# Optimization experiments

Hardware: AMD Instinct MI355X
Metric: run time of the kernel (lower is better)

Reference implementation:

```python
import jax, jax.numpy as jnp
import numpy as np

GROUPS = 4
KLD_SCALE = 10.0
COMMIT_COST = 0.25


def setup_inputs() -> dict:
    key = jax.random.key(0)
    k1, k2, k3, k4 = jax.random.split(key, 4)
    B, H, C = 8, 4096, 512
    n_embed, d = 512, C // GROUPS
    return {
        "z": jax.random.normal(k1, (B, H, C), dtype=jnp.float32),
        "embed_w": jax.random.normal(k2, (n_embed, d), dtype=jnp.float32),
        "proj_w": jax.random.normal(k3, (C, C), dtype=jnp.float32) * (1.0 / np.sqrt(C)),
        "proj_b": jax.random.normal(k4, (C,), dtype=jnp.float32) * 0.01,
    }


def reference(z, embed_w, proj_w, proj_b):
    B, H, C = z.shape
    d = C // GROUPS
    sg = jax.lax.stop_gradient
    # split channels into groups -> [B, H*groups, d]
    z_e = z.reshape(B, H * GROUPS, d)
    flat = z_e.reshape(-1, d)  # [N, d]
    dist = ((flat ** 2).sum(1, keepdims=True)
            - 2.0 * flat @ embed_w.T
            + (embed_w ** 2).sum(1)[None, :])  # [N, n_embed]
    ind = jnp.argmin(dist, axis=1).reshape(B, H * GROUPS)  # (-dist).max == dist.min
    z_q = embed_w[ind]  # [B, H*groups, d]
    diff = KLD_SCALE * (COMMIT_COST * jnp.mean((sg(z_q) - z_e) ** 2)
                        + jnp.mean((z_q - sg(z_e)) ** 2))
    # straight-through estimator
    z_q = z_e + sg(z_q - z_e)
    z_q = z_q.reshape(B, H, C)
    out = z_q @ proj_w.T + proj_b
    return out, diff, ind
```

## Files before the change

### kernel.cpp

```cpp
#include <hip/hip_runtime.h>

constexpr int D         = 128;
constexpr int NE        = 512;
constexpr int NROWS     = 131072;
constexpr int CC        = 512;
constexpr int OUT_ELEMS = 16777216;


using half8  = __attribute__((ext_vector_type(8))) _Float16;
using f32x16 = __attribute__((ext_vector_type(16))) float;

#define F16_MINNORM 6.103515625e-05f

__global__ void eprep_kernel(const float* __restrict__ embed,
                             unsigned short* __restrict__ esw,
                             float* __restrict__ entab,
                             float* __restrict__ ws_diff) {
    const int chunk = blockIdx.x;
    const int tid = threadIdx.x;
    const int cl = tid >> 3;
    const int seg = tid & 7;
    const float* src = embed + (size_t)(chunk * 32 + cl) * D + seg * 16;
    unsigned short* cb = esw + (size_t)chunk * 8192;

    float ss = 0.f;
#pragma unroll
    for (int g2 = 0; g2 < 2; g2++) {
        float4 a = ((const float4*)src)[g2 * 2 + 0];
        float4 b = ((const float4*)src)[g2 * 2 + 1];
        float v[8] = {a.x, a.y, a.z, a.w, b.x, b.y, b.z, b.w};
        half8 t1, t2;
#pragma unroll
        for (int i = 0; i < 8; i++) {
            ss += v[i] * v[i];
            float m2 = -2.0f * v[i];
            float m2c = (__builtin_fabsf(m2) < F16_MINNORM) ? 0.0f : m2;
            _Float16 h = (_Float16)m2c;
            float r = m2 - (float)h;
            t1[i] = h;
            t2[i] = (_Float16)(r * 2048.0f);
        }
        const int idx = seg * 512 + g2 * 256 + cl * 8;
        *(half8*)(cb + idx) = t1;
        *(half8*)(cb + 4096 + idx) = t2;
    }
    ss += __shfl_down(ss, 4, 8);
    ss += __shfl_down(ss, 2, 8);
    ss += __shfl_down(ss, 1, 8);
    if (seg == 0) entab[chunk * 32 + cl] = ss;
    if (chunk == 0 && tid == 0) ws_diff[0] = 0.0f;
}

#define AS_STRIDE 68
#define AS_S4 17

__launch_bounds__(256, 4)
__global__ void pgemm_kernel(const float* __restrict__ embed,
                             const float* __restrict__ projw,
                             float* __restrict__ P) {
    __shared__ float As[64 * AS_STRIDE];
    __shared__ float Bs[64 * AS_STRIDE];
    const int tid = threadIdx.x;
    const int cbase = blockIdx.x * 64;
    const int jbase = blockIdx.y * 64;
    const int g = blockIdx.z;
    const int tx = tid & 15, ty = tid >> 4;
    const int r = tid >> 2, seg = tid & 3;

    float acc[4][4];
#pragma unroll
    for (int i = 0; i < 4; i++)
#pragma unroll
        for (int j = 0; j < 4; j++) acc[i][j] = 0.f;

    for (int kb = 0; kb < D; kb += 64) {
        const float4* asrc = (const float4*)(embed + (size_t)(jbase + r) * D + kb + seg * 16);
        const float4* bsrc = (const float4*)(projw + (size_t)(cbase + r) * CC + g * D + kb + seg * 16);
        float4* adst = (float4*)&As[r * AS_STRIDE + seg * 16];
        float4* bdst = (float4*)&Bs[r * AS_STRIDE + seg * 16];
#pragma unroll
        for (int q = 0; q < 4; q++) { adst[q] = asrc[q]; bdst[q] = bsrc[q]; }
        __syncthreads();

        const float4* as4 = (const float4*)As;
        const float4* bs4 = (const float4*)Bs;
#pragma unroll 4
        for (int kk = 0; kk < 16; kk++) {
            float4 a[4], b[4];
#pragma unroll
            for (int i = 0; i < 4; i++) a[i] = as4[(ty + 16 * i) * AS_S4 + kk];
#pragma unroll
            for (int j = 0; j < 4; j++) b[j] = bs4[(tx + 16 * j) * AS_S4 + kk];
#pragma unroll
            for (int i = 0; i < 4; i++)
#pragma unroll
                for (int j = 0; j < 4; j++)
                    acc[i][j] += a[i].x * b[j].x + a[i].y * b[j].y +
                                 a[i].z * b[j].z + a[i].w * b[j].w;
        }
        __syncthreads();
    }
#pragma unroll
    for (int j = 0; j < 4; j++) {
#pragma unroll
        for (int i = 0; i < 4; i++)
            P[(size_t)g * 262144 + (size_t)(jbase + ty + 16 * i) * CC + cbase + tx + 16 * j] =
                acc[i][j];
    }
}

__global__ __launch_bounds__(256, 3)
void argmin_fused_kernel(const float* __restrict__ z,
                         const unsigned short* __restrict__ esw,
                         const float* __restrict__ entab,
                         const float* __restrict__ P,
                         const float* __restrict__ projb,
                         float* __restrict__ ws_diff,
                         float* __restrict__ ind_f,
                         float* __restrict__ out) {
    __shared__ unsigned char ebuf[32768];
    __shared__ int ind_s[128];
    const int tid = threadIdx.x;
    const int lane = tid & 63;
    const int wave = tid >> 6;
    const int h5 = lane >> 5, l5 = lane & 31;
    const int rb = blockIdx.x * 128 + wave * 32;

    half8 x1[8], x2[8];
    float xn = 0.f;
    {
        const float* zr = z + (size_t)(rb + l5) * D + h5 * 8;
#pragma unroll
        for (int kk = 0; kk < 8; kk++) {
            float4 a = *(const float4*)(zr + kk * 16);
            float4 b = *(const float4*)(zr + kk * 16 + 4);
            float v[8] = {a.x, a.y, a.z, a.w, b.x, b.y, b.z, b.w};
            half8 t1, t2;
#pragma unroll
            for (int i = 0; i < 8; i++) {
                xn += v[i] * v[i];
                float vc = (__builtin_fabsf(v[i]) < F16_MINNORM) ? 0.0f : v[i];
                _Float16 h = (_Float16)vc;
                float r = v[i] - (float)h;
                t1[i] = h;
                t2[i] = (_Float16)(r * 2048.0f);
            }
            x1[kk] = t1; x2[kk] = t2;
        }
    }

    float minv = 3.0e38f;
    int   mini = 0;

    auto stage = [&](int c, int b) {
        const unsigned char* s = (const unsigned char*)esw + (size_t)c * 16384 +
                                 wave * 4096 + lane * 16;
        unsigned char* d = &ebuf[b * 16384 + wave * 4096];
#pragma unroll
        for (int it = 0; it < 4; it++)
            __builtin_amdgcn_global_load_lds(
                (const __attribute__((address_space(1))) unsigned int*)(s + it * 1024),
                (__attribute__((address_space(3))) unsigned int*)(d + it * 1024),
                16, 0, 0);
    };

    stage(0, 0);
    __syncthreads();

#pragma unroll 1
    for (int c = 0; c < 16; c++) {
        if (c < 15) stage(c + 1, (c + 1) & 1);
        const unsigned char* ldsb = &ebuf[(c & 1) * 16384];

        float4 enr[4];
#pragma unroll
        for (int u = 0; u < 4; u++)
            enr[u] = *(const float4*)(entab + c * 32 + h5 * 4 + u * 8);

        f32x16 accA = (f32x16)(0.0f), accB = (f32x16)(0.0f);
#pragma unroll
        for (int kk = 0; kk < 8; kk++) {
            const int fo = kk * 1024 + h5 * 512 + l5 * 16;
            half8 e1 = *(const half8*)(ldsb + fo);
            half8 e2 = *(const half8*)(ldsb + 8192 + fo);
            accA = __builtin_amdgcn_mfma_f32_32x32x16_f16(e1, x1[kk], accA, 0, 0, 0);
            accB = __builtin_amdgcn_mfma_f32_32x32x16_f16(e1, x2[kk], accB, 0, 0, 0);
            accB = __builtin_amdgcn_mfma_f32_32x32x16_f16(e2, x1[kk], accB, 0, 0, 0);
        }

        const int cb2 = c * 32 + h5 * 4;
#pragma unroll
        for (int r = 0; r < 16; r++) {
            const float en = ((const float*)&enr[r >> 2])[r & 3];
            const int cand = cb2 + (r & 3) + 8 * (r >> 2);
            float d0 = fmaf(accB[r], 4.8828125e-4f, accA[r]) + en;
            if (d0 < minv) { minv = d0; mini = cand; }
        }
        __syncthreads();
    }

    {
        float ov = __shfl_xor(minv, 32);
        int oi = __shfl_xor(mini, 32);
        if (ov < minv || (ov == minv && oi < mini)) { minv = ov; mini = oi; }
    }
    if (lane < 32) {
        ind_f[rb + l5] = (float)mini;
        ind_s[wave * 32 + l5] = mini;
    }

    float xfull = xn + __shfl_xor(xn, 32);
    float v = (lane < 32) ? (xfull + minv) : 0.0f;
#pragma unroll
    for (int off = 32; off; off >>= 1) v += __shfl_down(v, off);
    if (lane == 0) atomicAdd(ws_diff, v);

    __syncthreads();

    const int mb = blockIdx.x * 32;
    const int c4 = tid & 127;
    const int mh = (tid >> 7) * 16;
    const float4 bias = ((const float4*)projb)[c4];
    const float4* P4 = (const float4*)P;
#pragma unroll 4
    for (int u = 0; u < 16; u++) {
        const int ml = mh + u;
        float4 acc = bias;
#pragma unroll
        for (int g = 0; g < 4; g++) {
            const int ig = ind_s[ml * 4 + g];
            float4 p = P4[(size_t)g * 65536 + (size_t)ig * 128 + c4];
            acc.x += p.x; acc.y += p.y; acc.z += p.z; acc.w += p.w;
        }
        ((float4*)out)[(size_t)(mb + ml) * 128 + c4] = acc;
    }
}

__global__ void finalize_kernel(const float* __restrict__ ws_diff,
                                float* __restrict__ diff_out) {
    diff_out[0] = 12.5f * ws_diff[0] * (1.0f / 16777216.0f);
}

extern "C" void kernel_launch(void* const* d_in, const int* in_sizes, int n_in,
                              void* d_out, int out_size, void* d_ws, size_t ws_size,
                              hipStream_t stream) {
    const float* z     = (const float*)d_in[0];
    const float* embed = (const float*)d_in[1];
    const float* projw = (const float*)d_in[2];
    const float* projb = (const float*)d_in[3];

    float* out      = (float*)d_out;
    float* diff_out = out + OUT_ELEMS;
    float* ind_f    = out + OUT_ELEMS + 1;

    char* wsb = (char*)d_ws;
    float* ws_diff = (float*)wsb;
    float* entab = (float*)(wsb + 1024);
    unsigned short* esw = (unsigned short*)(wsb + 4096);
    float* P = (float*)(wsb + 266240);

    eprep_kernel<<<16, 256, 0, stream>>>(embed, esw, entab, ws_diff);
    pgemm_kernel<<<dim3(8, 8, 4), 256, 0, stream>>>(embed, projw, P);
    argmin_fused_kernel<<<NROWS / 128, 256, 0, stream>>>(z, esw, entab, P, projb,
                                                         ws_diff, ind_f, out);
    finalize_kernel<<<1, 1, 0, stream>>>(ws_diff, diff_out);
}
```

Measured before the change: 218.2 us.

## Merge prep kernels, drop LDS codebook staging, fold finalize into main kernel

Combines the codebook-prep and P-GEMM launches into one grid and removes the separate finalize kernel by having the last block (via an atomic counter) write the diff scalar. The argmin kernel now reads the fp16 codebook directly from global/L2 into registers with one-step software prefetch, instead of staging through double-buffered LDS with block barriers. The output gather uses per-wave shuffles of indices rather than shared memory and a block sync. This cuts launch count and barriers and frees LDS for occupancy, at the cost of more global/L2 traffic for codebook reads and a threadfence/atomic tail.

```diff
diff --git a/kernel.cpp b/kernel.cpp
--- a/kernel.cpp
+++ b/kernel.cpp
@@ -12,58 +12,61 @@
 
 #define F16_MINNORM 6.103515625e-05f
 
-__global__ void eprep_kernel(const float* __restrict__ embed,
-                             unsigned short* __restrict__ esw,
-                             float* __restrict__ entab,
-                             float* __restrict__ ws_diff) {
-    const int chunk = blockIdx.x;
-    const int tid = threadIdx.x;
-    const int cl = tid >> 3;
-    const int seg = tid & 7;
-    const float* src = embed + (size_t)(chunk * 32 + cl) * D + seg * 16;
-    unsigned short* cb = esw + (size_t)chunk * 8192;
-
-    float ss = 0.f;
-#pragma unroll
-    for (int g2 = 0; g2 < 2; g2++) {
-        float4 a = ((const float4*)src)[g2 * 2 + 0];
-        float4 b = ((const float4*)src)[g2 * 2 + 1];
-        float v[8] = {a.x, a.y, a.z, a.w, b.x, b.y, b.z, b.w};
-        half8 t1, t2;
-#pragma unroll
-        for (int i = 0; i < 8; i++) {
-            ss += v[i] * v[i];
-            float m2 = -2.0f * v[i];
-            float m2c = (__builtin_fabsf(m2) < F16_MINNORM) ? 0.0f : m2;
-            _Float16 h = (_Float16)m2c;
-            float r = m2 - (float)h;
-            t1[i] = h;
-            t2[i] = (_Float16)(r * 2048.0f);
-        }
-        const int idx = seg * 512 + g2 * 256 + cl * 8;
-        *(half8*)(cb + idx) = t1;
-        *(half8*)(cb + 4096 + idx) = t2;
-    }
-    ss += __shfl_down(ss, 4, 8);
-    ss += __shfl_down(ss, 2, 8);
-    ss += __shfl_down(ss, 1, 8);
-    if (seg == 0) entab[chunk * 32 + cl] = ss;
-    if (chunk == 0 && tid == 0) ws_diff[0] = 0.0f;
-}
-
 #define AS_STRIDE 68
 #define AS_S4 17
 
 __launch_bounds__(256, 4)
-__global__ void pgemm_kernel(const float* __restrict__ embed,
-                             const float* __restrict__ projw,
-                             float* __restrict__ P) {
+__global__ void prep_kernel(const float* __restrict__ embed,
+                            const float* __restrict__ projw,
+                            unsigned short* __restrict__ esw,
+                            float* __restrict__ entab,
+                            float* __restrict__ ws_diff,
+                            unsigned int* __restrict__ ws_cnt,
+                            float* __restrict__ P) {
     __shared__ float As[64 * AS_STRIDE];
     __shared__ float Bs[64 * AS_STRIDE];
     const int tid = threadIdx.x;
-    const int cbase = blockIdx.x * 64;
-    const int jbase = blockIdx.y * 64;
-    const int g = blockIdx.z;
+
+    if (blockIdx.x >= 256) {
+        const int chunk = blockIdx.x - 256;
+        const int cl = tid >> 3;
+        const int seg = tid & 7;
+        const float* src = embed + (size_t)(chunk * 32 + cl) * D + seg * 16;
+        unsigned short* cb = esw + (size_t)chunk * 8192;
+
+        float ss = 0.f;
+#pragma unroll
+        for (int g2 = 0; g2 < 2; g2++) {
+            float4 a = ((const float4*)src)[g2 * 2 + 0];
+            float4 b = ((const float4*)src)[g2 * 2 + 1];
+            float v[8] = {a.x, a.y, a.z, a.w, b.x, b.y, b.z, b.w};
+            half8 t1, t2;
+#pragma unroll
+            for (int i = 0; i < 8; i++) {
+                ss += v[i] * v[i];
+                float m2 = -2.0f * v[i];
+                float m2c = (__builtin_fabsf(m2) < F16_MINNORM) ? 0.0f : m2;
+                _Float16 h = (_Float16)m2c;
+                float r = m2 - (float)h;
+                t1[i] = h;
+                t2[i] = (_Float16)(r * 2048.0f);
+            }
+            const int idx = seg * 512 + g2 * 256 + cl * 8;
+            *(half8*)(cb + idx) = t1;
+            *(half8*)(cb + 4096 + idx) = t2;
+        }
+        ss += __shfl_down(ss, 4, 8);
+        ss += __shfl_down(ss, 2, 8);
+        ss += __shfl_down(ss, 1, 8);
+        if (seg == 0) entab[chunk * 32 + cl] = ss;
+        if (chunk == 0 && tid == 0) { ws_diff[0] = 0.0f; ws_cnt[0] = 0u; }
+        return;
+    }
+
+    const int b = blockIdx.x;
+    const int cbase = (b & 7) * 64;
+    const int jbase = ((b >> 3) & 7) * 64;
+    const int g = b >> 6;
     const int tx = tid & 15, ty = tid >> 4;
     const int r = tid >> 2, seg = tid & 3;
 
@@ -86,17 +89,17 @@
         const float4* bs4 = (const float4*)Bs;
 #pragma unroll 4
         for (int kk = 0; kk < 16; kk++) {
-            float4 a[4], b[4];
+            float4 a[4], bb[4];
 #pragma unroll
             for (int i = 0; i < 4; i++) a[i] = as4[(ty + 16 * i) * AS_S4 + kk];
 #pragma unroll
-            for (int j = 0; j < 4; j++) b[j] = bs4[(tx + 16 * j) * AS_S4 + kk];
+            for (int j = 0; j < 4; j++) bb[j] = bs4[(tx + 16 * j) * AS_S4 + kk];
 #pragma unroll
             for (int i = 0; i < 4; i++)
 #pragma unroll
                 for (int j = 0; j < 4; j++)
-                    acc[i][j] += a[i].x * b[j].x + a[i].y * b[j].y +
-                                 a[i].z * b[j].z + a[i].w * b[j].w;
+                    acc[i][j] += a[i].x * bb[j].x + a[i].y * bb[j].y +
+                                 a[i].z * bb[j].z + a[i].w * bb[j].w;
         }
         __syncthreads();
     }
@@ -116,10 +119,10 @@
                          const float* __restrict__ P,
                          const float* __restrict__ projb,
                          float* __restrict__ ws_diff,
+                         unsigned int* __restrict__ ws_cnt,
                          float* __restrict__ ind_f,
-                         float* __restrict__ out) {
-    __shared__ unsigned char ebuf[32768];
-    __shared__ int ind_s[128];
+                         float* __restrict__ out,
+                         float* __restrict__ diff_out) {
     const int tid = threadIdx.x;
     const int lane = tid & 63;
     const int wave = tid >> 6;
@@ -152,25 +155,13 @@
     float minv = 3.0e38f;
     int   mini = 0;
 
-    auto stage = [&](int c, int b) {
-        const unsigned char* s = (const unsigned char*)esw + (size_t)c * 16384 +
-                                 wave * 4096 + lane * 16;
-        unsigned char* d = &ebuf[b * 16384 + wave * 4096];
-#pragma unroll
-        for (int it = 0; it < 4; it++)
-            __builtin_amdgcn_global_load_lds(
-                (const __attribute__((address_space(1))) unsigned int*)(s + it * 1024),
-                (__attribute__((address_space(3))) unsigned int*)(d + it * 1024),
-                16, 0, 0);
-    };
-
-    stage(0, 0);
-    __syncthreads();
+    const unsigned char* ebase = (const unsigned char*)esw + h5 * 512 + l5 * 16;
+    half8 e1c = *(const half8*)(ebase);
+    half8 e2c = *(const half8*)(ebase + 8192);
 
 #pragma unroll 1
     for (int c = 0; c < 16; c++) {
-        if (c < 15) stage(c + 1, (c + 1) & 1);
-        const unsigned char* ldsb = &ebuf[(c & 1) * 16384];
+        const unsigned char* cb = ebase + (size_t)c * 16384;
 
         float4 enr[4];
 #pragma unroll
@@ -180,12 +171,14 @@
         f32x16 accA = (f32x16)(0.0f), accB = (f32x16)(0.0f);
 #pragma unroll
         for (int kk = 0; kk < 8; kk++) {
-            const int fo = kk * 1024 + h5 * 512 + l5 * 16;
-            half8 e1 = *(const half8*)(ldsb + fo);
-            half8 e2 = *(const half8*)(ldsb + 8192 + fo);
-            accA = __builtin_amdgcn_mfma_f32_32x32x16_f16(e1, x1[kk], accA, 0, 0, 0);
-            accB = __builtin_amdgcn_mfma_f32_32x32x16_f16(e1, x2[kk], accB, 0, 0, 0);
-            accB = __builtin_amdgcn_mfma_f32_32x32x16_f16(e2, x1[kk], accB, 0, 0, 0);
+            const unsigned char* np =
+                cb + ((kk < 7) ? (kk + 1) * 1024 : (c < 15 ? 16384 : 0));
+            half8 n1 = *(const half8*)(np);
+            half8 n2 = *(const half8*)(np + 8192);
+            accA = __builtin_amdgcn_mfma_f32_32x32x16_f16(e1c, x1[kk], accA, 0, 0, 0);
+            accB = __builtin_amdgcn_mfma_f32_32x32x16_f16(e1c, x2[kk], accB, 0, 0, 0);
+            accB = __builtin_amdgcn_mfma_f32_32x32x16_f16(e2c, x1[kk], accB, 0, 0, 0);
+            e1c = n1; e2c = n2;
         }
 
         const int cb2 = c * 32 + h5 * 4;
@@ -196,7 +189,6 @@
             float d0 = fmaf(accB[r], 4.8828125e-4f, accA[r]) + en;
             if (d0 < minv) { minv = d0; mini = cand; }
         }
-        __syncthreads();
     }
 
     {
@@ -204,41 +196,50 @@
         int oi = __shfl_xor(mini, 32);
         if (ov < minv || (ov == minv && oi < mini)) { minv = ov; mini = oi; }
     }
-    if (lane < 32) {
-        ind_f[rb + l5] = (float)mini;
-        ind_s[wave * 32 + l5] = mini;
-    }
+    if (lane < 32) ind_f[rb + l5] = (float)mini;
 
     float xfull = xn + __shfl_xor(xn, 32);
     float v = (lane < 32) ? (xfull + minv) : 0.0f;
 #pragma unroll
     for (int off = 32; off; off >>= 1) v += __shfl_down(v, off);
-    if (lane == 0) atomicAdd(ws_diff, v);
-
-    __syncthreads();
-
-    const int mb = blockIdx.x * 32;
-    const int c4 = tid & 127;
-    const int mh = (tid >> 7) * 16;
-    const float4 bias = ((const float4*)projb)[c4];
-    const float4* P4 = (const float4*)P;
-#pragma unroll 4
-    for (int u = 0; u < 16; u++) {
-        const int ml = mh + u;
-        float4 acc = bias;
-#pragma unroll
-        for (int g = 0; g < 4; g++) {
-            const int ig = ind_s[ml * 4 + g];
-            float4 p = P4[(size_t)g * 65536 + (size_t)ig * 128 + c4];
-            acc.x += p.x; acc.y += p.y; acc.z += p.z; acc.w += p.w;
-        }
-        ((float4*)out)[(size_t)(mb + ml) * 128 + c4] = acc;
-    }
-}
-
-__global__ void finalize_kernel(const float* __restrict__ ws_diff,
-                                float* __restrict__ diff_out) {
-    diff_out[0] = 12.5f * ws_diff[0] * (1.0f / 16777216.0f);
+    if (lane == 0) {
+        atomicAdd(ws_diff, v);
+        __threadfence();
+        unsigned t = atomicAdd(ws_cnt, 1u);
+        if (t == 4095u) {
+            __threadfence();
+            float s = atomicAdd(ws_diff, 0.0f);
+            diff_out[0] = 12.5f * s * (1.0f / 16777216.0f);
+        }
+    }
+
+    const int ob = rb >> 2;
+    const float4* P4  = (const float4*)P;
+    const float4* pb4 = (const float4*)projb;
+    float4* out4 = (float4*)out;
+    const float4 bias0 = pb4[lane];
+    const float4 bias1 = pb4[64 + lane];
+#pragma unroll 2
+    for (int r = 0; r < 8; r++) {
+        const int ig0 = __shfl(mini, r * 4 + 0);
+        const int ig1 = __shfl(mini, r * 4 + 1);
+        const int ig2 = __shfl(mini, r * 4 + 2);
+        const int ig3 = __shfl(mini, r * 4 + 3);
+#pragma unroll
+        for (int p = 0; p < 2; p++) {
+            const int c4 = p * 64 + lane;
+            float4 acc = p ? bias1 : bias0;
+            float4 a0 = P4[(size_t)ig0 * 128 + c4];
+            float4 a1 = P4[ 65536 + (size_t)ig1 * 128 + c4];
+            float4 a2 = P4[131072 + (size_t)ig2 * 128 + c4];
+            float4 a3 = P4[196608 + (size_t)ig3 * 128 + c4];
+            acc.x += a0.x + a1.x + a2.x + a3.x;
+            acc.y += a0.y + a1.y + a2.y + a3.y;
+            acc.z += a0.z + a1.z + a2.z + a3.z;
+            acc.w += a0.w + a1.w + a2.w + a3.w;
+            out4[(size_t)(ob + r) * 128 + c4] = acc;
+        }
+    }
 }
 
 extern "C" void kernel_launch(void* const* d_in, const int* in_sizes, int n_in,
@@ -255,13 +256,13 @@
 
     char* wsb = (char*)d_ws;
     float* ws_diff = (float*)wsb;
+    unsigned int* ws_cnt = (unsigned int*)(wsb + 512);
     float* entab = (float*)(wsb + 1024);
     unsigned short* esw = (unsigned short*)(wsb + 4096);
     float* P = (float*)(wsb + 266240);
 
-    eprep_kernel<<<16, 256, 0, stream>>>(embed, esw, entab, ws_diff);
-    pgemm_kernel<<<dim3(8, 8, 4), 256, 0, stream>>>(embed, projw, P);
+    prep_kernel<<<272, 256, 0, stream>>>(embed, projw, esw, entab, ws_diff, ws_cnt, P);
     argmin_fused_kernel<<<NROWS / 128, 256, 0, stream>>>(z, esw, entab, P, projb,
-                                                         ws_diff, ind_f, out);
-    finalize_kernel<<<1, 1, 0, stream>>>(ws_diff, diff_out);
+                                                         ws_diff, ws_cnt, ind_f, out,
+                                                         diff_out);
 }
```

Result: slower. 316.9 us (+45.3%).
